# Kernel tuning notes

Hardware: AMD Instinct MI355X
Metric: run time of the kernel (lower is better)

The kernel has to match this reference:

```python
import jax, jax.numpy as jnp
import numpy as np

DIM = 256
K = 2048
B = 256
C = 10.0  # logit clipping constant


def setup_inputs() -> dict:
    key = jax.random.key(0)
    ks = jax.random.split(key, 7)
    bound = 1.0 / np.sqrt(DIM)
    return {
        "encoder_output": jax.random.normal(ks[0], (K, B, DIM), dtype=jnp.float32),
        "query": jax.random.normal(ks[1], (B, DIM), dtype=jnp.float32),
        # w_q: nn.Linear(dim, dim)
        "Wq": jax.random.uniform(ks[2], (DIM, DIM), jnp.float32, -bound, bound),
        "bq": jax.random.uniform(ks[3], (DIM,), jnp.float32, -bound, bound),
        # w_ref: nn.Conv1d(dim, dim, 1) == per-position linear over channels
        "Wref": jax.random.uniform(ks[4], (DIM, DIM), jnp.float32, -bound, bound),
        "bref": jax.random.uniform(ks[5], (DIM,), jnp.float32, -bound, bound),
        # v parameter, uniform(-1/sqrt(dim), 1/sqrt(dim))
        "v": jax.random.uniform(ks[6], (DIM,), jnp.float32, -bound, bound),
    }


def reference(encoder_output, query, Wq, bq, Wref, bref, v):
    # encoder_output: (k, B, dim); query: (B, dim)
    # q = w_q(query) -> (B, dim)
    q = query @ Wq.T + bq
    # ref = Conv1d(dim,dim,1) applied to encoder_output.permute(1,2,0) -> (B, dim, k)
    ref = jnp.einsum('kbe,de->bdk', encoder_output, Wref) + bref[None, :, None]
    # u[b,i] = sum_d v[d] * tanh(ref[b,d,i] + q[b,d])  -> (B, k)
    u = jnp.einsum('d,bdk->bk', v, jnp.tanh(ref + q[:, :, None]))
    # use_logit_clip=True
    logit = C * jnp.tanh(u)
    return logit
```

## Files before the change

### kernel.cpp

```cpp
#include <hip/hip_runtime.h>

#define DIM   256
#define KSEQ  2048
#define BATCH 256
#define NROWS (KSEQ * BATCH)
#define NSTRIPS (NROWS / 32)

typedef __attribute__((ext_vector_type(8))) __bf16 bf16x8;
typedef __attribute__((ext_vector_type(4))) float  floatx4;
typedef __attribute__((ext_vector_type(8))) short  short8;

__device__ __forceinline__ unsigned short f2bf_bits(float f) {
    unsigned u = __builtin_bit_cast(unsigned, f);
    u += 0x7fffu + ((u >> 16) & 1u);
    return (unsigned short)(u >> 16);
}

__device__ __forceinline__ __bf16 f2bf(float f) {
    return __builtin_bit_cast(__bf16, f2bf_bits(f));
}

__device__ __forceinline__ float fast_tanh(float x) {
    float e = __expf(2.0f * x);
    return 1.0f - 2.0f * __builtin_amdgcn_rcpf(e + 1.0f);
}

__global__ void qpb_kernel(const float* __restrict__ query,
                           const float* __restrict__ Wq,
                           const float* __restrict__ bq,
                           const float* __restrict__ bref,
                           float* __restrict__ qpb) {
    __shared__ float qs[DIM];
    const int b = blockIdx.x;
    const int d = threadIdx.x;
    qs[d] = query[b * DIM + d];
    __syncthreads();
    const float* wrow = Wq + d * DIM;
    float acc = 0.f;
#pragma unroll 8
    for (int e = 0; e < DIM; ++e) acc += qs[e] * wrow[e];
    qpb[b * DIM + d] = acc + bq[d] + bref[d];
}

__global__ __launch_bounds__(1024) void attn_kernel(
        const float* __restrict__ enc,
        const float* __restrict__ qpb,
        const float* __restrict__ Wref,
        const float* __restrict__ v,
        float* __restrict__ out) {
    __shared__ short wlds[DIM * DIM];

    const int tid = threadIdx.x;

#pragma unroll
    for (int it = 0; it < 8; ++it) {
        const int flat = it * 1024 + tid;
        const int d = flat >> 5;
        const int c = flat & 31;
        const float* src = Wref + d * DIM + c * 8;
        float4 f0 = *(const float4*)(src);
        float4 f1 = *(const float4*)(src + 4);
        short8 sv;
        sv[0] = (short)f2bf_bits(f0.x); sv[1] = (short)f2bf_bits(f0.y);
        sv[2] = (short)f2bf_bits(f0.z); sv[3] = (short)f2bf_bits(f0.w);
        sv[4] = (short)f2bf_bits(f1.x); sv[5] = (short)f2bf_bits(f1.y);
        sv[6] = (short)f2bf_bits(f1.z); sv[7] = (short)f2bf_bits(f1.w);
        *(short8*)&wlds[d * DIM + ((c ^ (d & 15)) << 3)] = sv;
    }
    __syncthreads();

    const int lane = tid & 63;
    const int wave = tid >> 6;
    const int n = lane & 15;
    const int g = lane >> 4;

    for (int strip = blockIdx.x * 16 + wave; strip < NSTRIPS; strip += 256 * 16) {
        const int rowbase = strip * 32;

        bf16x8 afrag[2][8];
#pragma unroll
        for (int m = 0; m < 2; ++m) {
            const float* rowp = enc + (size_t)(rowbase + m * 16 + n) * DIM + g * 8;
#pragma unroll
            for (int s = 0; s < 8; ++s) {
                float4 f0 = *(const float4*)(rowp + s * 32);
                float4 f1 = *(const float4*)(rowp + s * 32 + 4);
                bf16x8 a;
                a[0] = f2bf(f0.x); a[1] = f2bf(f0.y); a[2] = f2bf(f0.z); a[3] = f2bf(f0.w);
                a[4] = f2bf(f1.x); a[5] = f2bf(f1.y); a[6] = f2bf(f1.z); a[7] = f2bf(f1.w);
                afrag[m][s] = a;
            }
        }

        float u[2][4] = {{0.f, 0.f, 0.f, 0.f}, {0.f, 0.f, 0.f, 0.f}};
        const int bbase = rowbase & 255;
        const float* qbase = qpb + (size_t)bbase * DIM;

        for (int t = 0; t < 16; ++t) {
            const int d = t * 16 + n;
            floatx4 acc0 = {0.f, 0.f, 0.f, 0.f};
            floatx4 acc1 = {0.f, 0.f, 0.f, 0.f};
#pragma unroll
            for (int s = 0; s < 8; ++s) {
                short8 raw = *(const short8*)&wlds[(t * 16 + n) * DIM +
                                                   (((s * 4 + g) ^ n) << 3)];
                bf16x8 bfrag = __builtin_bit_cast(bf16x8, raw);
                acc0 = __builtin_amdgcn_mfma_f32_16x16x32_bf16(afrag[0][s], bfrag, acc0, 0, 0, 0);
                acc1 = __builtin_amdgcn_mfma_f32_16x16x32_bf16(afrag[1][s], bfrag, acc1, 0, 0, 0);
            }
            const float vd = v[d];
#pragma unroll
            for (int rg = 0; rg < 4; ++rg) {
                const int r0 = (g * 4 + rg) * DIM;
                const int r1 = (16 + g * 4 + rg) * DIM;
                float x0 = acc0[rg] + qbase[r0 + d];
                float x1 = acc1[rg] + qbase[r1 + d];
                u[0][rg] += vd * fast_tanh(x0);
                u[1][rg] += vd * fast_tanh(x1);
            }
        }

#pragma unroll
        for (int m = 0; m < 2; ++m) {
#pragma unroll
            for (int rg = 0; rg < 4; ++rg) {
                float s = u[m][rg];
                s += __shfl_xor(s, 1);
                s += __shfl_xor(s, 2);
                s += __shfl_xor(s, 4);
                s += __shfl_xor(s, 8);
                if (n == 0) {
                    const int r = rowbase + m * 16 + g * 4 + rg;
                    out[(size_t)(r & 255) * KSEQ + (r >> 8)] = 10.0f * fast_tanh(s);
                }
            }
        }
    }
}

extern "C" void kernel_launch(void* const* d_in, const int* in_sizes, int n_in,
                              void* d_out, int out_size, void* d_ws, size_t ws_size,
                              hipStream_t stream) {
    const float* enc   = (const float*)d_in[0];
    const float* query = (const float*)d_in[1];
    const float* Wq    = (const float*)d_in[2];
    const float* bq    = (const float*)d_in[3];
    const float* Wref  = (const float*)d_in[4];
    const float* bref  = (const float*)d_in[5];
    const float* v     = (const float*)d_in[6];
    float* out = (float*)d_out;
    float* qpb = (float*)d_ws;

    qpb_kernel<<<BATCH, DIM, 0, stream>>>(query, Wq, bq, bref, qpb);
    attn_kernel<<<256, 1024, 0, stream>>>(enc, qpb, Wref, v, out);
}
```

Baseline: 820.9 us.

## Widen strips to four M-tiles, transpose qpb, hoist v into registers

Each wave now handles 64 rows (four 16-row MFMA tiles) per strip, so every LDS B-fragment load feeds four MFMAs instead of two. The q+bias buffer is stored transposed so the four per-lane q values come from one float4 load instead of scattered loads, and v is cached in registers. Blocks shrink to 512 threads with a target of two blocks per CU. The cost is much higher register pressure from holding 32 A-fragments plus a fully unrolled t loop, which could force spills or cut occupancy. With 64 KB of LDS per block, two blocks per CU also depends on the LDS capacity.

```diff
diff --git a/kernel.cpp b/kernel.cpp
--- a/kernel.cpp
+++ b/kernel.cpp
@@ -4,7 +4,12 @@
 #define KSEQ  2048
 #define BATCH 256
 #define NROWS (KSEQ * BATCH)
-#define NSTRIPS (NROWS / 32)
+#define MTILES 4
+#define STRIPROWS (MTILES * 16)
+#define NSTRIPS (NROWS / STRIPROWS)
+#define BLOCKS 256
+#define WAVES_PER_BLOCK 8
+#define TOTALWAVES (BLOCKS * WAVES_PER_BLOCK)
 
 typedef __attribute__((ext_vector_type(8))) __bf16 bf16x8;
 typedef __attribute__((ext_vector_type(4))) float  floatx4;
@@ -29,7 +34,7 @@
                            const float* __restrict__ Wq,
                            const float* __restrict__ bq,
                            const float* __restrict__ bref,
-                           float* __restrict__ qpb) {
+                           float* __restrict__ qpbT) {
     __shared__ float qs[DIM];
     const int b = blockIdx.x;
     const int d = threadIdx.x;
@@ -39,12 +44,12 @@
     float acc = 0.f;
 #pragma unroll 8
     for (int e = 0; e < DIM; ++e) acc += qs[e] * wrow[e];
-    qpb[b * DIM + d] = acc + bq[d] + bref[d];
+    qpbT[d * BATCH + b] = acc + bq[d] + bref[d];
 }
 
-__global__ __launch_bounds__(1024) void attn_kernel(
+__global__ __launch_bounds__(512, 2) void attn_kernel(
         const float* __restrict__ enc,
-        const float* __restrict__ qpb,
+        const float* __restrict__ qpbT,
         const float* __restrict__ Wref,
         const float* __restrict__ v,
         float* __restrict__ out) {
@@ -53,8 +58,8 @@
     const int tid = threadIdx.x;
 
 #pragma unroll
-    for (int it = 0; it < 8; ++it) {
-        const int flat = it * 1024 + tid;
+    for (int it = 0; it < 16; ++it) {
+        const int flat = it * 512 + tid;
         const int d = flat >> 5;
         const int c = flat & 31;
         const float* src = Wref + d * DIM + c * 8;
@@ -74,12 +79,19 @@
     const int n = lane & 15;
     const int g = lane >> 4;
 
-    for (int strip = blockIdx.x * 16 + wave; strip < NSTRIPS; strip += 256 * 16) {
-        const int rowbase = strip * 32;
+    float vreg[16];
+#pragma unroll
+    for (int t = 0; t < 16; ++t) vreg[t] = v[t * 16 + n];
 
-        bf16x8 afrag[2][8];
+    for (int strip = blockIdx.x * WAVES_PER_BLOCK + wave; strip < NSTRIPS;
+         strip += TOTALWAVES) {
+        const int rowbase = strip * STRIPROWS;
+        const int bbase = rowbase & 255;
+        const float* qbase = qpbT + bbase + g * 4;
+
+        bf16x8 afrag[MTILES][8];
 #pragma unroll
-        for (int m = 0; m < 2; ++m) {
+        for (int m = 0; m < MTILES; ++m) {
             const float* rowp = enc + (size_t)(rowbase + m * 16 + n) * DIM + g * 8;
 #pragma unroll
             for (int s = 0; s < 8; ++s) {
@@ -92,36 +104,41 @@
             }
         }
 
-        float u[2][4] = {{0.f, 0.f, 0.f, 0.f}, {0.f, 0.f, 0.f, 0.f}};
-        const int bbase = rowbase & 255;
-        const float* qbase = qpb + (size_t)bbase * DIM;
+        float u[MTILES][4];
+#pragma unroll
+        for (int m = 0; m < MTILES; ++m)
+#pragma unroll
+            for (int rg = 0; rg < 4; ++rg) u[m][rg] = 0.f;
 
+#pragma unroll
         for (int t = 0; t < 16; ++t) {
             const int d = t * 16 + n;
-            floatx4 acc0 = {0.f, 0.f, 0.f, 0.f};
-            floatx4 acc1 = {0.f, 0.f, 0.f, 0.f};
+            floatx4 acc[MTILES];
+#pragma unroll
+            for (int m = 0; m < MTILES; ++m) acc[m] = (floatx4){0.f, 0.f, 0.f, 0.f};
 #pragma unroll
             for (int s = 0; s < 8; ++s) {
-                short8 raw = *(const short8*)&wlds[(t * 16 + n) * DIM +
-                                                   (((s * 4 + g) ^ n) << 3)];
+                short8 raw = *(const short8*)&wlds[d * DIM + (((s * 4 + g) ^ n) << 3)];
                 bf16x8 bfrag = __builtin_bit_cast(bf16x8, raw);
-                acc0 = __builtin_amdgcn_mfma_f32_16x16x32_bf16(afrag[0][s], bfrag, acc0, 0, 0, 0);
-                acc1 = __builtin_amdgcn_mfma_f32_16x16x32_bf16(afrag[1][s], bfrag, acc1, 0, 0, 0);
+#pragma unroll
+                for (int m = 0; m < MTILES; ++m)
+                    acc[m] = __builtin_amdgcn_mfma_f32_16x16x32_bf16(
+                        afrag[m][s], bfrag, acc[m], 0, 0, 0);
             }
-            const float vd = v[d];
+            const float vd = vreg[t];
+            const float* qrow = qbase + (size_t)d * BATCH;
 #pragma unroll
-            for (int rg = 0; rg < 4; ++rg) {
-                const int r0 = (g * 4 + rg) * DIM;
-                const int r1 = (16 + g * 4 + rg) * DIM;
-                float x0 = acc0[rg] + qbase[r0 + d];
-                float x1 = acc1[rg] + qbase[r1 + d];
-                u[0][rg] += vd * fast_tanh(x0);
-                u[1][rg] += vd * fast_tanh(x1);
+            for (int m = 0; m < MTILES; ++m) {
+                float4 qf = *(const float4*)(qrow + m * 16);
+                u[m][0] += vd * fast_tanh(acc[m][0] + qf.x);
+                u[m][1] += vd * fast_tanh(acc[m][1] + qf.y);
+                u[m][2] += vd * fast_tanh(acc[m][2] + qf.z);
+                u[m][3] += vd * fast_tanh(acc[m][3] + qf.w);
             }
         }
 
 #pragma unroll
-        for (int m = 0; m < 2; ++m) {
+        for (int m = 0; m < MTILES; ++m) {
 #pragma unroll
             for (int rg = 0; rg < 4; ++rg) {
                 float s = u[m][rg];
@@ -148,9 +165,9 @@
     const float* Wref  = (const float*)d_in[4];
     const float* bref  = (const float*)d_in[5];
     const float* v     = (const float*)d_in[6];
-    float* out = (float*)d_out;
-    float* qpb = (float*)d_ws;
+    float* out  = (float*)d_out;
+    float* qpbT = (float*)d_ws;
 
-    qpb_kernel<<<BATCH, DIM, 0, stream>>>(query, Wq, bq, bref, qpb);
-    attn_kernel<<<256, 1024, 0, stream>>>(enc, qpb, Wref, v, out);
+    qpb_kernel<<<BATCH, DIM, 0, stream>>>(query, Wq, bq, bref, qpbT);
+    attn_kernel<<<BLOCKS, 512, 0, stream>>>(enc, qpbT, Wref, v, out);
 }
```

After: 1.997 ms. +143.2%, slower.
